# Kernel optimization log

Hardware: AMD Instinct MI355X
Metric: run time of the kernel (lower is better)

## Reference

```python
import jax, jax.numpy as jnp
import numpy as np

B, T, C, H = 4, 2048, 1024, 16
HS = C // H  # head_size = 64
EPS = 1e-5


def setup_inputs() -> dict:
    key = jax.random.key(0)
    ks = jax.random.split(key, 16)
    s = 0.02
    inp = {
        "x": jax.random.normal(ks[0], (B, T, C), jnp.float32),
        # custom LayerNorm buffers (gamma=ones, beta=zeros in source)
        "ln1_g": jnp.ones((C,), jnp.float32),
        "ln1_b": jnp.zeros((C,), jnp.float32),
        "ln2_g": jnp.ones((C,), jnp.float32),
        "ln2_b": jnp.zeros((C,), jnp.float32),
        # per-head Q/K/V linears, stacked over heads: [H, C, HS]
        "Wq": jax.random.normal(ks[1], (H, C, HS), jnp.float32) * s,
        "bq": jax.random.normal(ks[2], (H, HS), jnp.float32) * s,
        "Wk": jax.random.normal(ks[3], (H, C, HS), jnp.float32) * s,
        "bk": jax.random.normal(ks[4], (H, HS), jnp.float32) * s,
        "Wv": jax.random.normal(ks[5], (H, C, HS), jnp.float32) * s,
        "bv": jax.random.normal(ks[6], (H, HS), jnp.float32) * s,
        # output projection [C, C]
        "Wo": jax.random.normal(ks[7], (C, C), jnp.float32) * s,
        "bo": jax.random.normal(ks[8], (C,), jnp.float32) * s,
        # FFN: C -> 4C -> C
        "W1": jax.random.normal(ks[9], (C, 4 * C), jnp.float32) * s,
        "b1": jax.random.normal(ks[10], (4 * C,), jnp.float32) * s,
        "W2": jax.random.normal(ks[11], (4 * C, C), jnp.float32) * s,
        "b2": jax.random.normal(ks[12], (C,), jnp.float32) * s,
    }
    return inp


def _layernorm_time_axis(x, g, b):
    # Faithful to source: normalizes over axis=1 (time), unbiased variance (ddof=1).
    m = jnp.mean(x, axis=1, keepdims=True)
    v = jnp.var(x, axis=1, keepdims=True, ddof=1)
    return g * (x - m) / jnp.sqrt(v + EPS) + b


def reference(x, ln1_g, ln1_b, ln2_g, ln2_b, Wq, bq, Wk, bk, Wv, bv, Wo, bo, W1, b1, W2, b2):
    Bc, Tc, Cc = x.shape
    h = _layernorm_time_axis(x, ln1_g, ln1_b)
    # per-head projections: [B, H, T, HS]
    q = jnp.einsum('btc,hcd->bhtd', h, Wq) + bq[None, :, None, :]
    k = jnp.einsum('btc,hcd->bhtd', h, Wk) + bk[None, :, None, :]
    v = jnp.einsum('btc,hcd->bhtd', h, Wv) + bv[None, :, None, :]
    # scores scaled by C**-0.5 (full embed dim, as in source)
    wei = jnp.einsum('bhtd,bhsd->bhts', q, k) * (Cc ** -0.5)
    causal = jnp.tril(jnp.ones((Tc, Tc), bool))
    wei = jnp.where(causal[None, None], wei, -jnp.inf)
    wei = jax.nn.softmax(wei, axis=-1)
    att = jnp.einsum('bhts,bhsd->bhtd', wei, v)
    # concat heads -> [B, T, C], then projection
    att = att.transpose(0, 2, 1, 3).reshape(Bc, Tc, Cc)
    x = x + att @ Wo + bo
    # FFN on ln2
    h2 = _layernorm_time_axis(x, ln2_g, ln2_b)
    ff = jax.nn.relu(h2 @ W1 + b1) @ W2 + b2
    return x + ff
```

## Files before the change

### kernel.cpp

```cpp
#include <hip/hip_runtime.h>

#define B_   4
#define T_   2048
#define C_   1024
#define H_   16
#define HS_  64
#define BT_  (B_*T_)
#define EPS_ 1e-5f

typedef unsigned short u16;
typedef unsigned int   u32;
typedef __attribute__((ext_vector_type(8))) __bf16 bf16x8;
typedef __attribute__((ext_vector_type(4))) float  f32x4;
typedef __attribute__((ext_vector_type(8))) u16    u16x8;
typedef __attribute__((ext_vector_type(4))) u16    u16x4;
typedef __attribute__((ext_vector_type(4))) u32    u32x4;

__device__ __forceinline__ u16 f2bf(float f) {
  unsigned x = __builtin_bit_cast(unsigned, f);
  x += 0x7fffu + ((x >> 16) & 1u);
  return (u16)(x >> 16);
}
__device__ __forceinline__ float bf2f(u16 v) {
  return __builtin_bit_cast(float, (u32)v << 16);
}

__device__ __forceinline__ float fast_exp2(float x) {
  float y;
  asm("v_exp_f32 %0, %1" : "=v"(y) : "v"(x));
  return y;
}
__device__ __forceinline__ float fast_rcp(float x) {
  float y;
  asm("v_rcp_f32 %0, %1" : "=v"(y) : "v"(x));
  return y;
}

#define GLD_LDS16(src, dst) \
  __builtin_amdgcn_global_load_lds((__attribute__((address_space(1))) void*)(src), \
                                   (__attribute__((address_space(3))) void*)(dst), 16, 0, 0)

__global__ __launch_bounds__(256) void ln_partial(const float* __restrict__ x,
                                                  float* __restrict__ ps,
                                                  float* __restrict__ psq) {
  int col = blockIdx.x * 256 + threadIdx.x;
  int b = col >> 10, c = col & (C_ - 1);
  int t0 = blockIdx.y * (T_ / 16);
  const float* p = x + (size_t)b * T_ * C_ + (size_t)t0 * C_ + c;
  float s = 0.f, sq = 0.f;
  #pragma unroll 4
  for (int i = 0; i < T_ / 16; ++i) { float v = p[(size_t)i * C_]; s += v; sq += v * v; }
  ps [blockIdx.y * (B_ * C_) + col] = s;
  psq[blockIdx.y * (B_ * C_) + col] = sq;
}

__global__ __launch_bounds__(256) void ln_partial_bf(const u16* __restrict__ x,
                                                     float* __restrict__ ps,
                                                     float* __restrict__ psq) {
  int col = blockIdx.x * 256 + threadIdx.x;
  int b = col >> 10, c = col & (C_ - 1);
  int t0 = blockIdx.y * (T_ / 16);
  const u16* p = x + (size_t)b * T_ * C_ + (size_t)t0 * C_ + c;
  float s = 0.f, sq = 0.f;
  #pragma unroll 4
  for (int i = 0; i < T_ / 16; ++i) { float v = bf2f(p[(size_t)i * C_]); s += v; sq += v * v; }
  ps [blockIdx.y * (B_ * C_) + col] = s;
  psq[blockIdx.y * (B_ * C_) + col] = sq;
}

__global__ __launch_bounds__(256) void ln_final(const float* __restrict__ ps,
                                                const float* __restrict__ psq,
                                                float* __restrict__ mean,
                                                float* __restrict__ rstd) {
  int col = blockIdx.x * 256 + threadIdx.x;
  float s = 0.f, sq = 0.f;
  #pragma unroll
  for (int i = 0; i < 16; ++i) { s += ps[i * (B_ * C_) + col]; sq += psq[i * (B_ * C_) + col]; }
  float m = s * (1.f / T_);
  float var = (sq - (float)T_ * m * m) * (1.f / (T_ - 1));
  mean[col] = m;
  rstd[col] = rsqrtf(var + EPS_);
}

__global__ __launch_bounds__(256) void ln_norm(const float* __restrict__ x,
                                               const float* __restrict__ mean,
                                               const float* __restrict__ rstd,
                                               const float* __restrict__ gam,
                                               const float* __restrict__ bet,
                                               u16* __restrict__ out) {
  size_t i = ((size_t)blockIdx.x * 256 + threadIdx.x) * 4;
  int c  = (int)(i & (C_ - 1));
  int b  = (int)(i >> 21);
  int bc = (b << 10) + c;
  float4 v = *(const float4*)(x + i);
  float vv[4] = {v.x, v.y, v.z, v.w};
  u16x4 o;
  #pragma unroll
  for (int j = 0; j < 4; ++j)
    o[j] = f2bf(gam[c + j] * (vv[j] - mean[bc + j]) * rstd[bc + j] + bet[c + j]);
  *(u16x4*)(out + i) = o;
}

__global__ __launch_bounds__(256) void ln_norm_bf(const u16* __restrict__ x,
                                                  const float* __restrict__ mean,
                                                  const float* __restrict__ rstd,
                                                  const float* __restrict__ gam,
                                                  const float* __restrict__ bet,
                                                  u16* __restrict__ out) {
  size_t i = ((size_t)blockIdx.x * 256 + threadIdx.x) * 4;
  int c  = (int)(i & (C_ - 1));
  int b  = (int)(i >> 21);
  int bc = (b << 10) + c;
  u16x4 v = *(const u16x4*)(x + i);
  u16x4 o;
  #pragma unroll
  for (int j = 0; j < 4; ++j)
    o[j] = f2bf(gam[c + j] * (bf2f(v[j]) - mean[bc + j]) * rstd[bc + j] + bet[c + j]);
  *(u16x4*)(out + i) = o;
}

__global__ __launch_bounds__(256) void transpose_cast(const float* __restrict__ in,
                                                      u16* __restrict__ out,
                                                      int cols_in, int ld_out,
                                                      size_t batch_in, size_t batch_out) {
  __shared__ float tile[32][33];
  const float* I = in + (size_t)blockIdx.z * batch_in;
  u16* Ou = out + (size_t)blockIdx.z * batch_out;
  int r0 = blockIdx.y << 5, c0 = blockIdx.x << 5;
  int tx = threadIdx.x & 31, ty = threadIdx.x >> 5;
  #pragma unroll
  for (int rr = 0; rr < 32; rr += 8)
    tile[ty + rr][tx] = I[(size_t)(r0 + ty + rr) * cols_in + c0 + tx];
  __syncthreads();
  #pragma unroll
  for (int rr = 0; rr < 32; rr += 8)
    Ou[(size_t)(c0 + ty + rr) * ld_out + r0 + tx] = f2bf(tile[tx][ty + rr]);
}

__global__ __launch_bounds__(256) void concat_bias(const float* __restrict__ bq,
                                                   const float* __restrict__ bk,
                                                   const float* __restrict__ bv,
                                                   float* __restrict__ out) {
  int i = blockIdx.x * 256 + threadIdx.x;
  float v = (i < 1024) ? bq[i] : (i < 2048 ? bk[i - 1024] : bv[i - 2048]);
  out[i] = v;
}

__global__ __launch_bounds__(256) void v_transpose(const u16* __restrict__ qkv,
                                                   u16* __restrict__ Vt) {
  __shared__ u16 tile[32][33];
  int bh = blockIdx.z; int b = bh >> 4, h = bh & 15;
  int t0 = blockIdx.x << 5, hs0 = blockIdx.y << 5;
  int tx = threadIdx.x & 31, ty = threadIdx.x >> 5;
  const u16* src = qkv + (size_t)(b * T_ + t0) * 3072 + 2048 + h * 64 + hs0;
  #pragma unroll
  for (int rr = 0; rr < 32; rr += 8)
    tile[ty + rr][tx] = src[(size_t)(ty + rr) * 3072 + tx];
  __syncthreads();
  u16* dst = Vt + ((size_t)bh * 64 + hs0) * T_ + t0;
  #pragma unroll
  for (int rr = 0; rr < 32; rr += 8)
    dst[(size_t)(ty + rr) * T_ + tx] = tile[tx][ty + rr];
}

template<int RELU, int QSCALE>
__global__ __launch_bounds__(256, 2)
void gemm_128x256(const u16* __restrict__ A,
                  const u16* __restrict__ Bt,
                  const float* __restrict__ bias,
                  u16* __restrict__ outp,
                  int M, int N, int K) {
  constexpr int BK = 32;
  __shared__ u16 sA[3][128 * BK];
  __shared__ u16 sB[3][256 * BK];

  const int tid = threadIdx.x;
  const int wave = tid >> 6, lane = tid & 63;
  const int g = lane >> 4, r16 = lane & 15;

  const int nbx = N >> 8;
  const int nwg = gridDim.x;
  const int bid = blockIdx.x;
  const int swz = ((bid & 7) * (nwg >> 3)) + (bid >> 3);
  const int bx = swz % nbx, by = swz / nbx;
  const int row0 = by << 7, col0 = bx << 8;

  const u16* aS[2];
  const u16* bS[4];
  #pragma unroll
  for (int j = 0; j < 2; ++j) {
    const int ci = tid + 256 * j, row = ci >> 2, cc = ci & 3;
    aS[j] = A + (size_t)(row0 + row) * K + ((cc ^ ((row >> 1) & 3)) * 8);
  }
  #pragma unroll
  for (int j = 0; j < 4; ++j) {
    const int ci = tid + 256 * j, row = ci >> 2, cc = ci & 3;
    bS[j] = Bt + (size_t)(col0 + row) * K + ((cc ^ ((row >> 1) & 3)) * 8);
  }
  const int ldsOff = wave * 512;

  auto stage = [&](int t, int buf) {
    const int ko = t * BK;
    #pragma unroll
    for (int j = 0; j < 2; ++j)
      GLD_LDS16(aS[j] + ko, &sA[buf][ldsOff + j * 2048]);
    #pragma unroll
    for (int j = 0; j < 4; ++j)
      GLD_LDS16(bS[j] + ko, &sB[buf][ldsOff + j * 2048]);
  };

  const int wrow = (wave >> 1) * 64;
  const int wcol = (wave & 1) * 128;
  f32x4 acc[4][8] = {};

  const int NT = K / BK;

  stage(0, 0); stage(1, 1);
  asm volatile("s_waitcnt vmcnt(6)" ::: "memory");
  __builtin_amdgcn_s_barrier();
  __builtin_amdgcn_sched_barrier(0);

  for (int t = 0; t < NT; ++t) {
    const u16* As = sA[t % 3];
    const u16* Bs = sB[t % 3];
    bf16x8 af[4], bf[8];
    #pragma unroll
    for (int m = 0; m < 4; ++m) {
      const int lr = wrow + m * 16 + r16;
      af[m] = *(const bf16x8*)&As[lr * 32 + ((g ^ ((lr >> 1) & 3)) * 8)];
    }
    #pragma unroll
    for (int n = 0; n < 8; ++n) {
      const int lr = wcol + n * 16 + r16;
      bf[n] = *(const bf16x8*)&Bs[lr * 32 + ((g ^ ((lr >> 1) & 3)) * 8)];
    }
    if (t + 2 < NT) stage(t + 2, (t + 2) % 3);

    __builtin_amdgcn_s_setprio(1);
    #pragma unroll
    for (int m = 0; m < 4; ++m)
      #pragma unroll
      for (int n = 0; n < 8; ++n)
        acc[m][n] = __builtin_amdgcn_mfma_f32_16x16x32_bf16(af[m], bf[n], acc[m][n], 0, 0, 0);
    __builtin_amdgcn_s_setprio(0);

    if (t + 1 < NT) {
      if (t + 2 < NT) asm volatile("s_waitcnt vmcnt(6)" ::: "memory");
      else            asm volatile("s_waitcnt vmcnt(0)" ::: "memory");
      __builtin_amdgcn_s_barrier();
      __builtin_amdgcn_sched_barrier(0);
    }
  }

  #pragma unroll
  for (int m = 0; m < 4; ++m) {
    #pragma unroll
    for (int n = 0; n < 8; ++n) {
      const int col = col0 + wcol + n * 16 + r16;
      const float bv = bias[col];
      const float sc = (QSCALE && col < 1024) ? 0.04508422003f : 1.f;
      const int rowb = row0 + wrow + m * 16 + g * 4;
      #pragma unroll
      for (int r = 0; r < 4; ++r) {
        float v = acc[m][n][r] + bv;
        if (RELU) v = fmaxf(v, 0.f);
        if (QSCALE) v *= sc;
        outp[(size_t)(rowb + r) * N + col] = f2bf(v);
      }
    }
  }
}

template<int RELU, int RAW, int QSCALE>
__global__ __launch_bounds__(512, 2)
void gemm_256(const u16* __restrict__ A,
              const u16* __restrict__ Bt,
              const float* __restrict__ bias,
              const u16* __restrict__ resb,
              void* __restrict__ outp,
              void* __restrict__ outp_b,
              int M, int N, int K) {
  constexpr int BK = 32;
  __shared__ u16 sA[4][256 * BK];
  __shared__ u16 sB[4][256 * BK];

  const int tid = threadIdx.x;
  const int wave = tid >> 6, lane = tid & 63;
  const int g = lane >> 4, r16 = lane & 15;

  const int nbx = N >> 8;
  const int nwg = gridDim.x;
  const int bid = blockIdx.x;
  const int swz = ((bid & 7) * (nwg >> 3)) + (bid >> 3);
  const int bx = swz % nbx, by = swz / nbx;
  const int row0 = by << 8, col0 = bx << 8;

  const int kspan = RAW ? (K >> 1) : K;
  const int kbase = RAW ? ((int)blockIdx.y * kspan) : 0;

  const u16* aS[2];
  const u16* bS[2];
  #pragma unroll
  for (int j = 0; j < 2; ++j) {
    const int ci = tid + 512 * j, row = ci >> 2, cc = ci & 3;
    aS[j] = A  + (size_t)(row0 + row) * K + ((cc ^ ((row >> 1) & 3)) * 8) + kbase;
    bS[j] = Bt + (size_t)(col0 + row) * K + ((cc ^ ((row >> 1) & 3)) * 8) + kbase;
  }
  const int ldsOff = wave * 512;

  auto stage = [&](int t, int buf) {
    const int ko = t * BK;
    #pragma unroll
    for (int j = 0; j < 2; ++j)
      GLD_LDS16(aS[j] + ko, &sA[buf][ldsOff + j * 4096]);
    #pragma unroll
    for (int j = 0; j < 2; ++j)
      GLD_LDS16(bS[j] + ko, &sB[buf][ldsOff + j * 4096]);
  };

  const int wrow = (wave >> 2) * 128;
  const int wcol = (wave & 3) * 64;
  f32x4 acc[8][4] = {};

  const int NT = kspan / BK;

  stage(0, 0); stage(1, 1);
  asm volatile("s_waitcnt vmcnt(4)" ::: "memory");
  __builtin_amdgcn_s_barrier();
  __builtin_amdgcn_sched_barrier(0);

  for (int t = 0; t < NT; ++t) {
    const u16* As = sA[t & 3];
    const u16* Bs = sB[t & 3];
    bf16x8 af[8], bf[4];

    #pragma unroll
    for (int m = 0; m < 4; ++m) {
      const int lr = wrow + m * 16 + r16;
      af[m] = *(const bf16x8*)&As[lr * 32 + ((g ^ ((lr >> 1) & 3)) * 8)];
    }
    #pragma unroll
    for (int n = 0; n < 4; ++n) {
      const int lr = wcol + n * 16 + r16;
      bf[n] = *(const bf16x8*)&Bs[lr * 32 + ((g ^ ((lr >> 1) & 3)) * 8)];
    }
    if (t + 2 < NT) stage(t + 2, (t + 2) & 3);

    __builtin_amdgcn_s_barrier();
    asm volatile("s_waitcnt lgkmcnt(0)" ::: "memory");
    __builtin_amdgcn_sched_barrier(0);
    __builtin_amdgcn_s_setprio(1);
    #pragma unroll
    for (int m = 0; m < 4; ++m)
      #pragma unroll
      for (int n = 0; n < 4; ++n)
        acc[m][n] = __builtin_amdgcn_mfma_f32_16x16x32_bf16(af[m], bf[n], acc[m][n], 0, 0, 0);
    __builtin_amdgcn_s_setprio(0);

    #pragma unroll
    for (int m = 4; m < 8; ++m) {
      const int lr = wrow + m * 16 + r16;
      af[m] = *(const bf16x8*)&As[lr * 32 + ((g ^ ((lr >> 1) & 3)) * 8)];
    }
    __builtin_amdgcn_s_barrier();
    asm volatile("s_waitcnt lgkmcnt(0)" ::: "memory");
    __builtin_amdgcn_sched_barrier(0);
    __builtin_amdgcn_s_setprio(1);
    #pragma unroll
    for (int m = 4; m < 8; ++m)
      #pragma unroll
      for (int n = 0; n < 4; ++n)
        acc[m][n] = __builtin_amdgcn_mfma_f32_16x16x32_bf16(af[m], bf[n], acc[m][n], 0, 0, 0);
    __builtin_amdgcn_s_setprio(0);

    if (t + 1 < NT) {
      if (t + 2 < NT) asm volatile("s_waitcnt vmcnt(4)" ::: "memory");
      else            asm volatile("s_waitcnt vmcnt(0)" ::: "memory");
      __builtin_amdgcn_s_barrier();
      __builtin_amdgcn_sched_barrier(0);
    }
  }

  if constexpr (RAW) {
    if (blockIdx.y) {
      float* po = (float*)outp_b;
      #pragma unroll
      for (int m = 0; m < 8; ++m) {
        #pragma unroll
        for (int n = 0; n < 4; ++n) {
          const int col = col0 + wcol + n * 16 + r16;
          const float bv = bias[col];
          const int rowb = row0 + wrow + m * 16 + g * 4;
          #pragma unroll
          for (int r = 0; r < 4; ++r) {
            const size_t idx = (size_t)(rowb + r) * N + col;
            po[idx] = acc[m][n][r] + bv + bf2f(resb[idx]);
          }
        }
      }
    } else {
      float* po = (float*)outp;
      #pragma unroll
      for (int m = 0; m < 8; ++m) {
        #pragma unroll
        for (int n = 0; n < 4; ++n) {
          const int col = col0 + wcol + n * 16 + r16;
          const int rowb = row0 + wrow + m * 16 + g * 4;
          #pragma unroll
          for (int r = 0; r < 4; ++r)
            po[(size_t)(rowb + r) * N + col] = acc[m][n][r];
        }
      }
    }
  } else {
    u16* po = (u16*)outp;
    #pragma unroll
    for (int m = 0; m < 8; ++m) {
      #pragma unroll
      for (int n = 0; n < 4; ++n) {
        const int col = col0 + wcol + n * 16 + r16;
        const float bv = bias[col];
        const float sc = (QSCALE && col < 1024) ? 0.04508422003f : 1.f;
        const int rowb = row0 + wrow + m * 16 + g * 4;
        #pragma unroll
        for (int r = 0; r < 4; ++r) {
          float v = acc[m][n][r] + bv;
          if (RELU) v = fmaxf(v, 0.f);
          if (QSCALE) v *= sc;
          po[(size_t)(rowb + r) * N + col] = f2bf(v);
        }
      }
    }
  }
}

__global__ __launch_bounds__(256) void ffn2_reduce(const float* __restrict__ pA,
                                                   float* __restrict__ out) {
  size_t i = ((size_t)blockIdx.x * 256 + threadIdx.x) * 4;
  float4 a = *(const float4*)(pA + i);
  float4 o = *(const float4*)(out + i);
  float4 v;
  v.x = a.x + o.x;
  v.y = a.y + o.y;
  v.z = a.z + o.z;
  v.w = a.w + o.w;
  *(float4*)(out + i) = v;
}

template<int BM, int BN, int THREADS, int OUT_F32, int RELU, int RES>
__global__ __launch_bounds__(THREADS, 3)
void gemm_pipe(const u16* __restrict__ A,
               const u16* __restrict__ Bt,
               const float* __restrict__ bias,
               const float* __restrict__ res,
               void* __restrict__ outp,
               int M, int N, int K) {
  constexpr int BK  = 32;
  constexpr int CHA = (BM * 4) / THREADS;
  constexpr int CHB = (BN * 4) / THREADS;
  constexpr int CH  = CHA + CHB;

  __shared__ u16 sA[3][BM * BK];
  __shared__ u16 sB[3][BN * BK];

  const int tid = threadIdx.x;
  const int wave = tid >> 6, lane = tid & 63;
  const int g = lane >> 4, r16 = lane & 15;

  const int nbx = N / BN;
  const int nwg = gridDim.x;
  const int bid = blockIdx.x;
  const int swz = ((bid & 7) * (nwg >> 3)) + (bid >> 3);
  const int bx = swz % nbx, by = swz / nbx;
  const int row0 = by * BM, col0 = bx * BN;

  const u16* aS[CHA];
  const u16* bS[CHB];
  #pragma unroll
  for (int j = 0; j < CHA; ++j) {
    const int ci = tid + THREADS * j, row = ci >> 2, cc = ci & 3;
    aS[j] = A + (size_t)(row0 + row) * K + ((cc ^ ((row >> 1) & 3)) * 8);
  }
  #pragma unroll
  for (int j = 0; j < CHB; ++j) {
    const int ci = tid + THREADS * j, row = ci >> 2, cc = ci & 3;
    bS[j] = Bt + (size_t)(col0 + row) * K + ((cc ^ ((row >> 1) & 3)) * 8);
  }
  const int ldsOff = wave * 512;

  auto stage = [&](int t, int buf) {
    const int ko = t * BK;
    #pragma unroll
    for (int j = 0; j < CHA; ++j)
      GLD_LDS16(aS[j] + ko, &sA[buf][ldsOff + j * (THREADS * 8)]);
    #pragma unroll
    for (int j = 0; j < CHB; ++j)
      GLD_LDS16(bS[j] + ko, &sB[buf][ldsOff + j * (THREADS * 8)]);
  };

  const int wrow = (wave >> 1) * 64;
  const int wcol = (wave & 1) * 64;
  f32x4 acc[4][4] = {};

  const int NT = K / BK;

  stage(0, 0); stage(1, 1);
  if constexpr (CH == 3) asm volatile("s_waitcnt vmcnt(3)" ::: "memory");
  else                   asm volatile("s_waitcnt vmcnt(4)" ::: "memory");
  __builtin_amdgcn_s_barrier();
  __builtin_amdgcn_sched_barrier(0);

  for (int t = 0; t < NT; ++t) {
    if (t + 2 < NT) stage(t + 2, (t + 2) % 3);
    const u16* As = sA[t % 3];
    const u16* Bs = sB[t % 3];
    bf16x8 af[4], bf[4];
    #pragma unroll
    for (int m = 0; m < 4; ++m) {
      const int lr = wrow + m * 16 + r16;
      af[m] = *(const bf16x8*)&As[lr * 32 + ((g ^ ((lr >> 1) & 3)) * 8)];
    }
    #pragma unroll
    for (int n = 0; n < 4; ++n) {
      const int lr = wcol + n * 16 + r16;
      bf[n] = *(const bf16x8*)&Bs[lr * 32 + ((g ^ ((lr >> 1) & 3)) * 8)];
    }
    __builtin_amdgcn_s_setprio(1);
    #pragma unroll
    for (int m = 0; m < 4; ++m)
      #pragma unroll
      for (int n = 0; n < 4; ++n)
        acc[m][n] = __builtin_amdgcn_mfma_f32_16x16x32_bf16(af[m], bf[n], acc[m][n], 0, 0, 0);
    __builtin_amdgcn_s_setprio(0);

    if (t + 1 < NT) {
      if (t + 2 < NT) {
        if constexpr (CH == 3) asm volatile("s_waitcnt vmcnt(3)" ::: "memory");
        else                   asm volatile("s_waitcnt vmcnt(4)" ::: "memory");
      } else {
        asm volatile("s_waitcnt vmcnt(0)" ::: "memory");
      }
      __builtin_amdgcn_s_barrier();
      __builtin_amdgcn_sched_barrier(0);
    }
  }

  #pragma unroll
  for (int m = 0; m < 4; ++m) {
    #pragma unroll
    for (int n = 0; n < 4; ++n) {
      const int col = col0 + wcol + n * 16 + r16;
      const float bv = bias[col];
      const int rowb = row0 + wrow + m * 16 + g * 4;
      #pragma unroll
      for (int r = 0; r < 4; ++r) {
        const size_t idx = (size_t)(rowb + r) * N + col;
        float v = acc[m][n][r] + bv;
        if (RES)  v += res[idx];
        if (RELU) v = fmaxf(v, 0.f);
        if (OUT_F32) ((float*)outp)[idx] = v;
        else         ((u16*)outp)[idx]   = f2bf(v);
      }
    }
  }
}

__global__ __launch_bounds__(256, 4) void attn_fwd(const u16* __restrict__ qkv,
                                                   const u16* __restrict__ Vt,
                                                   u16* __restrict__ O) {
  __shared__ u16 sK[2][64 * 64];
  __shared__ u16 sV[2][64 * 64];

  const int orig = blockIdx.x;
  const int work = ((orig & 7) << 7) + (orig >> 3);
  const int i = work & 15;
  const int h = (work >> 4) & 15;
  const int b = work >> 8;
  const int qA = i << 6, qB = (31 - i) << 6;
  const int nA = i + 1,  nB = 32 - i;

  const int tid = threadIdx.x, wave = tid >> 6, lane = tid & 63;
  const int g = lane >> 4, r16 = lane & 15;

  const size_t base = (size_t)b * T_ * 3072 + h * 64;
  const u16* Qp = qkv + base;
  const u16* Kp = qkv + base + 1024;
  const u16* VtP = Vt + (size_t)(b * 16 + h) * 64 * T_;

  const int rowL = lane >> 3;
  const int colL = 8 * ((lane & 7) ^ rowL);
  const u16* kSrc = Kp  + (size_t)(wave * 16 + rowL) * 3072 + colL;
  const u16* vSrc = VtP + (size_t)(wave * 16 + rowL) * T_   + colL;
  u16* kDst0 = &sK[0][(wave * 16 + 0) * 64];
  u16* kDst8 = &sK[0][(wave * 16 + 8) * 64];
  u16* vDst0 = &sV[0][(wave * 16 + 0) * 64];
  u16* vDst8 = &sV[0][(wave * 16 + 8) * 64];

  const int ck0 = (( 0 + g * 16) ^ ((r16 & 7) << 4)) >> 1;
  const int ck1 = ((64 + g * 16) ^ ((r16 & 7) << 4)) >> 1;

  bf16x8 qfA[2], qfB[2];
  #pragma unroll
  for (int kc = 0; kc < 2; ++kc) {
    qfA[kc] = *(const bf16x8*)(Qp + (size_t)(qA + wave * 16 + r16) * 3072 + kc * 32 + g * 8);
    qfB[kc] = *(const bf16x8*)(Qp + (size_t)(qB + wave * 16 + r16) * 3072 + kc * 32 + g * 8);
  }

  f32x4 accA[4] = {}, accB[4] = {};
  f32x4 lA4 = {}, lB4 = {};
  const int qaA = qA + wave * 16 + r16;
  const int qaB = qB + wave * 16 + r16;

  const u32 one2 = 0x3F803F80u;
  const u32x4 onesv = {one2, one2, one2, one2};
  const bf16x8 ONES = __builtin_bit_cast(bf16x8, onesv);

  int sbuf = 0;
  auto stageAdv = [&]() {
    const int o = sbuf * 4096;
    GLD_LDS16(kSrc,            kDst0 + o);
    GLD_LDS16(kSrc + 8 * 3072, kDst8 + o);
    GLD_LDS16(vSrc,            vDst0 + o);
    GLD_LDS16(vSrc + 8 * T_,   vDst8 + o);
    kSrc += 64 * 3072;
    vSrc += 64;
    sbuf ^= 1;
  };

  auto qkt = [&](const bf16x8* kf0, const bf16x8* kf1, const bf16x8* qf, f32x4* s) {
    __builtin_amdgcn_s_setprio(1);
    #pragma unroll
    for (int ni = 0; ni < 4; ++ni) {
      f32x4 t = {};
      t = __builtin_amdgcn_mfma_f32_16x16x32_bf16(kf0[ni], qf[0], t, 0, 0, 0);
      t = __builtin_amdgcn_mfma_f32_16x16x32_bf16(kf1[ni], qf[1], t, 0, 0, 0);
      s[ni] = t;
    }
    __builtin_amdgcn_s_setprio(0);
  };

  auto softmax_pack = [&](f32x4* s, bool diag, int q_abs, int kv0, bf16x8* pa) {
    if (diag) {
      #pragma unroll
      for (int ni = 0; ni < 4; ++ni)
        #pragma unroll
        for (int r = 0; r < 4; ++r) {
          const int kv_abs = kv0 + ni * 16 + g * 4 + r;
          if (kv_abs > q_abs) s[ni][r] = -3e38f;
        }
    }
    #pragma unroll
    for (int ni = 0; ni < 4; ++ni)
      #pragma unroll
      for (int r = 0; r < 4; ++r)
        s[ni][r] = fast_exp2(s[ni][r]);

    u32 pk[4][2];
    #pragma unroll
    for (int ni = 0; ni < 4; ++ni)
      #pragma unroll
      for (int h2 = 0; h2 < 2; ++h2)
        asm("v_cvt_pk_bf16_f32 %0, %1, %2"
            : "=v"(pk[ni][h2]) : "v"(s[ni][2 * h2]), "v"(s[ni][2 * h2 + 1]));

    u32 pa32[2][4];
    #pragma unroll
    for (int kc = 0; kc < 2; ++kc)
      #pragma unroll
      for (int h2 = 0; h2 < 2; ++h2) {
        u32 a = pk[2 * kc][h2], bq_ = pk[2 * kc + 1][h2];
        asm("v_permlane32_swap_b32 %0, %1" : "+v"(a), "+v"(bq_));
        asm("v_permlane16_swap_b32 %0, %1" : "+v"(a), "+v"(bq_));
        pa32[kc][h2] = a;
        pa32[kc][2 + h2] = bq_;
      }
    #pragma unroll
    for (int kc = 0; kc < 2; ++kc) {
      u32x4 tmp = {pa32[kc][0], pa32[kc][1], pa32[kc][2], pa32[kc][3]};
      pa[kc] = __builtin_bit_cast(bf16x8, tmp);
    }
  };

  stageAdv();
  asm volatile("s_waitcnt vmcnt(0)" ::: "memory");
  __builtin_amdgcn_s_barrier();
  __builtin_amdgcn_sched_barrier(0);

  int cbuf = 0;
  for (int t = 0; t < nB; ++t) {
    if (t + 1 < nB) stageAdv();
    const u16* Kb = sK[cbuf];
    const u16* Vb = sV[cbuf];
    const int kv0 = t << 6;
    const bool actA = (t < nA);

    bf16x8 kf0[4], kf1[4];
    #pragma unroll
    for (int ni = 0; ni < 4; ++ni) {
      kf0[ni] = *(const bf16x8*)&Kb[(ni * 16 + r16) * 64 + ck0];
      kf1[ni] = *(const bf16x8*)&Kb[(ni * 16 + r16) * 64 + ck1];
    }

    f32x4 s[4];
    bf16x8 paB[2], paA[2];

    qkt(kf0, kf1, qfB, s);
    softmax_pack(s, t == nB - 1, qaB, kv0, paB);
    if (actA) {
      qkt(kf0, kf1, qfA, s);
      softmax_pack(s, t == nA - 1, qaA, kv0, paA);
    }

    bf16x8 vf0[4], vf1[4];
    #pragma unroll
    for (int hsb = 0; hsb < 4; ++hsb) {
      vf0[hsb] = *(const bf16x8*)&Vb[(hsb * 16 + r16) * 64 + ck0];
      vf1[hsb] = *(const bf16x8*)&Vb[(hsb * 16 + r16) * 64 + ck1];
    }

    __builtin_amdgcn_s_setprio(1);
    lB4 = __builtin_amdgcn_mfma_f32_16x16x32_bf16(paB[0], ONES, lB4, 0, 0, 0);
    lB4 = __builtin_amdgcn_mfma_f32_16x16x32_bf16(paB[1], ONES, lB4, 0, 0, 0);
    #pragma unroll
    for (int hsb = 0; hsb < 4; ++hsb) {
      accB[hsb] = __builtin_amdgcn_mfma_f32_16x16x32_bf16(paB[0], vf0[hsb], accB[hsb], 0, 0, 0);
      accB[hsb] = __builtin_amdgcn_mfma_f32_16x16x32_bf16(paB[1], vf1[hsb], accB[hsb], 0, 0, 0);
    }
    if (actA) {
      lA4 = __builtin_amdgcn_mfma_f32_16x16x32_bf16(paA[0], ONES, lA4, 0, 0, 0);
      lA4 = __builtin_amdgcn_mfma_f32_16x16x32_bf16(paA[1], ONES, lA4, 0, 0, 0);
      #pragma unroll
      for (int hsb = 0; hsb < 4; ++hsb) {
        accA[hsb] = __builtin_amdgcn_mfma_f32_16x16x32_bf16(paA[0], vf0[hsb], accA[hsb], 0, 0, 0);
        accA[hsb] = __builtin_amdgcn_mfma_f32_16x16x32_bf16(paA[1], vf1[hsb], accA[hsb], 0, 0, 0);
      }
    }
    __builtin_amdgcn_s_setprio(0);

    if (t + 1 < nB) {
      asm volatile("s_waitcnt vmcnt(0)" ::: "memory");
      __builtin_amdgcn_s_barrier();
      __builtin_amdgcn_sched_barrier(0);
    }
    cbuf ^= 1;
  }

  float rlA[4], rlB[4];
  #pragma unroll
  for (int r = 0; r < 4; ++r) {
    rlA[r] = fast_rcp(lA4[r]);
    rlB[r] = fast_rcp(lB4[r]);
  }
  #pragma unroll
  for (int hsb = 0; hsb < 4; ++hsb)
    #pragma unroll
    for (int r = 0; r < 4; ++r) {
      const size_t rowA = (size_t)b * T_ + qA + wave * 16 + g * 4 + r;
      const size_t rowB = (size_t)b * T_ + qB + wave * 16 + g * 4 + r;
      O[rowA * C_ + h * 64 + hsb * 16 + r16] = f2bf(accA[hsb][r] * rlA[r]);
      O[rowB * C_ + h * 64 + hsb * 16 + r16] = f2bf(accB[hsb][r] * rlB[r]);
    }
}

extern "C" void kernel_launch(void* const* d_in, const int* in_sizes, int n_in,
                              void* d_out, int out_size, void* d_ws, size_t ws_size,
                              hipStream_t stream) {
  const float* x    = (const float*)d_in[0];
  const float* ln1g = (const float*)d_in[1];
  const float* ln1b = (const float*)d_in[2];
  const float* ln2g = (const float*)d_in[3];
  const float* ln2b = (const float*)d_in[4];
  const float* Wq   = (const float*)d_in[5];
  const float* bq   = (const float*)d_in[6];
  const float* Wk   = (const float*)d_in[7];
  const float* bk   = (const float*)d_in[8];
  const float* Wv   = (const float*)d_in[9];
  const float* bv   = (const float*)d_in[10];
  const float* Wo   = (const float*)d_in[11];
  const float* bo   = (const float*)d_in[12];
  const float* W1   = (const float*)d_in[13];
  const float* b1   = (const float*)d_in[14];
  const float* W2   = (const float*)d_in[15];
  const float* b2   = (const float*)d_in[16];

  char* w = (char*)d_ws;
  float* ps    = (float*)(w + 0);
  float* psq   = (float*)(w + 262144);
  float* mean  = (float*)(w + 524288);
  float* rstd  = (float*)(w + 540672);
  float* bqkv  = (float*)(w + 557056);
  u16*   h     = (u16*)  (w + 573440);
  u16*   wqkvT = (u16*)  (w + 17350656);
  u16*   woT   = (u16*)  (w + 23642112);
  u16*   w1T   = (u16*)  (w + 25739264);
  u16*   w2T   = (u16*)  (w + 34127872);
  u16*   x1b   = (u16*)  (w + 42516480);
  u16*   Vt    = (u16*)  (w + 59293696);
  u16*   qkv   = (u16*)  (w + 76070912);
  u16*   Oo    = (u16*)  (w + 126402560);
  u16*   u     = qkv;
  float* pA    = (float*)(w + 573440);

  transpose_cast<<<dim3(2, 32, 16), 256, 0, stream>>>(Wq, wqkvT,                     64,   1024, (size_t)C_ * 64, (size_t)64 * 1024);
  transpose_cast<<<dim3(2, 32, 16), 256, 0, stream>>>(Wk, wqkvT + (size_t)1024*1024, 64,   1024, (size_t)C_ * 64, (size_t)64 * 1024);
  transpose_cast<<<dim3(2, 32, 16), 256, 0, stream>>>(Wv, wqkvT + (size_t)2048*1024, 64,   1024, (size_t)C_ * 64, (size_t)64 * 1024);
  transpose_cast<<<dim3(32, 32, 1), 256, 0, stream>>>(Wo, woT, 1024, 1024, 0, 0);
  transpose_cast<<<dim3(128, 32, 1), 256, 0, stream>>>(W1, w1T, 4096, 1024, 0, 0);
  transpose_cast<<<dim3(32, 128, 1), 256, 0, stream>>>(W2, w2T, 1024, 4096, 0, 0);
  concat_bias<<<12, 256, 0, stream>>>(bq, bk, bv, bqkv);

  ln_partial<<<dim3(16, 16), 256, 0, stream>>>(x, ps, psq);
  ln_final<<<16, 256, 0, stream>>>(ps, psq, mean, rstd);
  ln_norm<<<8192, 256, 0, stream>>>(x, mean, rstd, ln1g, ln1b, h);

  gemm_128x256<0, 1><<<768, 256, 0, stream>>>(h, wqkvT, bqkv, qkv, BT_, 3072, 1024);

  v_transpose<<<dim3(T_ / 32, 2, B_ * H_), 256, 0, stream>>>(qkv, Vt);

  attn_fwd<<<1024, 256, 0, stream>>>(qkv, Vt, Oo);

  gemm_pipe<128, 128, 256, 0, 0, 1><<<512, 256, 0, stream>>>(Oo, woT, bo, x, x1b, BT_, 1024, 1024);

  ln_partial_bf<<<dim3(16, 16), 256, 0, stream>>>(x1b, ps, psq);
  ln_final<<<16, 256, 0, stream>>>(ps, psq, mean, rstd);
  ln_norm_bf<<<8192, 256, 0, stream>>>(x1b, mean, rstd, ln2g, ln2b, h);

  gemm_256<1, 0, 0><<<512, 512, 0, stream>>>(h, w1T, b1, nullptr, u, nullptr, BT_, 4096, 1024);
  gemm_256<0, 1, 0><<<dim3(128, 2), 512, 0, stream>>>(u, w2T, b2, x1b, pA, d_out, BT_, 1024, 4096);
  ffn2_reduce<<<8192, 256, 0, stream>>>(pA, (float*)d_out);
}
```

Measured before the change: 407.3 us.

## Add phased two-tile pipeline to gemm_256 and use 128x256 kernel for FFN1

Adds a PHASED variant of the 256x256 GEMM main loop that handles two K-tiles per iteration. Each half-tile of LDS fragment loads is split from its MFMA block by extra barriers, so loads and math interleave across waves in lockstep. The FFN down-projection now uses this variant. The FFN up-projection is moved to the existing 128x256 GEMM kernel with twice as many workgroups. The extra barriers add sync cost and assume an even tile count, which holds for K=4096.

```diff
diff --git a/kernel.cpp b/kernel.cpp
--- a/kernel.cpp
+++ b/kernel.cpp
@@ -271,7 +271,7 @@
   }
 }
 
-template<int RELU, int RAW, int QSCALE>
+template<int RELU, int RAW, int QSCALE, int PHASED>
 __global__ __launch_bounds__(512, 2)
 void gemm_256(const u16* __restrict__ A,
               const u16* __restrict__ Bt,
@@ -324,60 +324,145 @@
 
   const int NT = kspan / BK;
 
-  stage(0, 0); stage(1, 1);
-  asm volatile("s_waitcnt vmcnt(4)" ::: "memory");
-  __builtin_amdgcn_s_barrier();
-  __builtin_amdgcn_sched_barrier(0);
-
-  for (int t = 0; t < NT; ++t) {
-    const u16* As = sA[t & 3];
-    const u16* Bs = sB[t & 3];
-    bf16x8 af[8], bf[4];
-
-    #pragma unroll
-    for (int m = 0; m < 4; ++m) {
-      const int lr = wrow + m * 16 + r16;
-      af[m] = *(const bf16x8*)&As[lr * 32 + ((g ^ ((lr >> 1) & 3)) * 8)];
-    }
-    #pragma unroll
-    for (int n = 0; n < 4; ++n) {
-      const int lr = wcol + n * 16 + r16;
-      bf[n] = *(const bf16x8*)&Bs[lr * 32 + ((g ^ ((lr >> 1) & 3)) * 8)];
-    }
-    if (t + 2 < NT) stage(t + 2, (t + 2) & 3);
-
+  if constexpr (!PHASED) {
+    stage(0, 0); stage(1, 1);
+    asm volatile("s_waitcnt vmcnt(4)" ::: "memory");
     __builtin_amdgcn_s_barrier();
-    asm volatile("s_waitcnt lgkmcnt(0)" ::: "memory");
     __builtin_amdgcn_sched_barrier(0);
-    __builtin_amdgcn_s_setprio(1);
-    #pragma unroll
-    for (int m = 0; m < 4; ++m)
-      #pragma unroll
-      for (int n = 0; n < 4; ++n)
-        acc[m][n] = __builtin_amdgcn_mfma_f32_16x16x32_bf16(af[m], bf[n], acc[m][n], 0, 0, 0);
-    __builtin_amdgcn_s_setprio(0);
-
-    #pragma unroll
-    for (int m = 4; m < 8; ++m) {
-      const int lr = wrow + m * 16 + r16;
-      af[m] = *(const bf16x8*)&As[lr * 32 + ((g ^ ((lr >> 1) & 3)) * 8)];
-    }
+
+    for (int t = 0; t < NT; ++t) {
+      const u16* As = sA[t & 3];
+      const u16* Bs = sB[t & 3];
+      bf16x8 af[8], bf[4];
+      #pragma unroll
+      for (int m = 0; m < 8; ++m) {
+        const int lr = wrow + m * 16 + r16;
+        af[m] = *(const bf16x8*)&As[lr * 32 + ((g ^ ((lr >> 1) & 3)) * 8)];
+      }
+      #pragma unroll
+      for (int n = 0; n < 4; ++n) {
+        const int lr = wcol + n * 16 + r16;
+        bf[n] = *(const bf16x8*)&Bs[lr * 32 + ((g ^ ((lr >> 1) & 3)) * 8)];
+      }
+      if (t + 2 < NT) stage(t + 2, (t + 2) & 3);
+
+      __builtin_amdgcn_s_setprio(1);
+      #pragma unroll
+      for (int m = 0; m < 8; ++m)
+        #pragma unroll
+        for (int n = 0; n < 4; ++n)
+          acc[m][n] = __builtin_amdgcn_mfma_f32_16x16x32_bf16(af[m], bf[n], acc[m][n], 0, 0, 0);
+      __builtin_amdgcn_s_setprio(0);
+
+      if (t + 1 < NT) {
+        if (t + 2 < NT) asm volatile("s_waitcnt vmcnt(4)" ::: "memory");
+        else            asm volatile("s_waitcnt vmcnt(0)" ::: "memory");
+        __builtin_amdgcn_s_barrier();
+        __builtin_amdgcn_sched_barrier(0);
+      }
+    }
+  } else {
+    stage(0, 0); stage(1, 1);
+    asm volatile("s_waitcnt vmcnt(4)" ::: "memory");
     __builtin_amdgcn_s_barrier();
-    asm volatile("s_waitcnt lgkmcnt(0)" ::: "memory");
     __builtin_amdgcn_sched_barrier(0);
-    __builtin_amdgcn_s_setprio(1);
-    #pragma unroll
-    for (int m = 4; m < 8; ++m)
-      #pragma unroll
-      for (int n = 0; n < 4; ++n)
-        acc[m][n] = __builtin_amdgcn_mfma_f32_16x16x32_bf16(af[m], bf[n], acc[m][n], 0, 0, 0);
-    __builtin_amdgcn_s_setprio(0);
-
-    if (t + 1 < NT) {
+
+    for (int t = 0; t < NT; t += 2) {
+      const u16* As0 = sA[t & 3];
+      const u16* Bs0 = sB[t & 3];
+      const u16* As1 = sA[(t + 1) & 3];
+      const u16* Bs1 = sB[(t + 1) & 3];
+      bf16x8 af[8], bf[4];
+
+      #pragma unroll
+      for (int m = 0; m < 4; ++m) {
+        const int lr = wrow + m * 16 + r16;
+        af[m] = *(const bf16x8*)&As0[lr * 32 + ((g ^ ((lr >> 1) & 3)) * 8)];
+      }
+      #pragma unroll
+      for (int n = 0; n < 4; ++n) {
+        const int lr = wcol + n * 16 + r16;
+        bf[n] = *(const bf16x8*)&Bs0[lr * 32 + ((g ^ ((lr >> 1) & 3)) * 8)];
+      }
+      if (t + 2 < NT) stage(t + 2, (t + 2) & 3);
+      __builtin_amdgcn_s_barrier();
+      asm volatile("s_waitcnt lgkmcnt(0)" ::: "memory");
+      __builtin_amdgcn_sched_barrier(0);
+      __builtin_amdgcn_s_setprio(1);
+      #pragma unroll
+      for (int m = 0; m < 4; ++m)
+        #pragma unroll
+        for (int n = 0; n < 4; ++n)
+          acc[m][n] = __builtin_amdgcn_mfma_f32_16x16x32_bf16(af[m], bf[n], acc[m][n], 0, 0, 0);
+      __builtin_amdgcn_s_setprio(0);
+      __builtin_amdgcn_s_barrier();
+      __builtin_amdgcn_sched_barrier(0);
+
+      #pragma unroll
+      for (int m = 4; m < 8; ++m) {
+        const int lr = wrow + m * 16 + r16;
+        af[m] = *(const bf16x8*)&As0[lr * 32 + ((g ^ ((lr >> 1) & 3)) * 8)];
+      }
+      __builtin_amdgcn_s_barrier();
+      asm volatile("s_waitcnt lgkmcnt(0)" ::: "memory");
+      __builtin_amdgcn_sched_barrier(0);
+      __builtin_amdgcn_s_setprio(1);
+      #pragma unroll
+      for (int m = 4; m < 8; ++m)
+        #pragma unroll
+        for (int n = 0; n < 4; ++n)
+          acc[m][n] = __builtin_amdgcn_mfma_f32_16x16x32_bf16(af[m], bf[n], acc[m][n], 0, 0, 0);
+      __builtin_amdgcn_s_setprio(0);
       if (t + 2 < NT) asm volatile("s_waitcnt vmcnt(4)" ::: "memory");
       else            asm volatile("s_waitcnt vmcnt(0)" ::: "memory");
       __builtin_amdgcn_s_barrier();
       __builtin_amdgcn_sched_barrier(0);
+
+      #pragma unroll
+      for (int m = 0; m < 4; ++m) {
+        const int lr = wrow + m * 16 + r16;
+        af[m] = *(const bf16x8*)&As1[lr * 32 + ((g ^ ((lr >> 1) & 3)) * 8)];
+      }
+      #pragma unroll
+      for (int n = 0; n < 4; ++n) {
+        const int lr = wcol + n * 16 + r16;
+        bf[n] = *(const bf16x8*)&Bs1[lr * 32 + ((g ^ ((lr >> 1) & 3)) * 8)];
+      }
+      if (t + 3 < NT) stage(t + 3, (t + 3) & 3);
+      __builtin_amdgcn_s_barrier();
+      asm volatile("s_waitcnt lgkmcnt(0)" ::: "memory");
+      __builtin_amdgcn_sched_barrier(0);
+      __builtin_amdgcn_s_setprio(1);
+      #pragma unroll
+      for (int m = 0; m < 4; ++m)
+        #pragma unroll
+        for (int n = 0; n < 4; ++n)
+          acc[m][n] = __builtin_amdgcn_mfma_f32_16x16x32_bf16(af[m], bf[n], acc[m][n], 0, 0, 0);
+      __builtin_amdgcn_s_setprio(0);
+      __builtin_amdgcn_s_barrier();
+      __builtin_amdgcn_sched_barrier(0);
+
+      #pragma unroll
+      for (int m = 4; m < 8; ++m) {
+        const int lr = wrow + m * 16 + r16;
+        af[m] = *(const bf16x8*)&As1[lr * 32 + ((g ^ ((lr >> 1) & 3)) * 8)];
+      }
+      __builtin_amdgcn_s_barrier();
+      asm volatile("s_waitcnt lgkmcnt(0)" ::: "memory");
+      __builtin_amdgcn_sched_barrier(0);
+      __builtin_amdgcn_s_setprio(1);
+      #pragma unroll
+      for (int m = 4; m < 8; ++m)
+        #pragma unroll
+        for (int n = 0; n < 4; ++n)
+          acc[m][n] = __builtin_amdgcn_mfma_f32_16x16x32_bf16(af[m], bf[n], acc[m][n], 0, 0, 0);
+      __builtin_amdgcn_s_setprio(0);
+      if (t + 2 < NT) {
+        if (t + 3 < NT) asm volatile("s_waitcnt vmcnt(4)" ::: "memory");
+        else            asm volatile("s_waitcnt vmcnt(0)" ::: "memory");
+        __builtin_amdgcn_s_barrier();
+        __builtin_amdgcn_sched_barrier(0);
+      }
     }
   }
 
@@ -825,7 +910,7 @@
   ln_final<<<16, 256, 0, stream>>>(ps, psq, mean, rstd);
   ln_norm_bf<<<8192, 256, 0, stream>>>(x1b, mean, rstd, ln2g, ln2b, h);
 
-  gemm_256<1, 0, 0><<<512, 512, 0, stream>>>(h, w1T, b1, nullptr, u, nullptr, BT_, 4096, 1024);
-  gemm_256<0, 1, 0><<<dim3(128, 2), 512, 0, stream>>>(u, w2T, b2, x1b, pA, d_out, BT_, 1024, 4096);
+  gemm_128x256<1, 0><<<1024, 256, 0, stream>>>(h, w1T, b1, u, BT_, 4096, 1024);
+  gemm_256<0, 1, 0, 1><<<dim3(128, 2), 512, 0, stream>>>(u, w2T, b2, x1b, pA, d_out, BT_, 1024, 4096);
   ffn2_reduce<<<8192, 256, 0, stream>>>(pA, (float*)d_out);
 }
```

Measured after the change: 407.8 us. Within noise of the previous version (+0.1%).
